# Performance work log

Hardware: AMD Instinct MI355X
Metric: run time of the kernel (lower is better)

The kernel has to match this reference:

```python
import jax, jax.numpy as jnp
import numpy as np

B, I, DI, O, DO = 256, 1152, 8, 10, 16
ROUTING_ITERS = 3


def squash(s):
    # squash along last dim (out_capsule_dim); keepdims version of the
    # module's intended math: v = s * |s|^2 / (1+|s|^2) / |s|
    sq = jnp.sum(s * s, axis=-1, keepdims=True)
    return s * sq / (1.0 + sq) / jnp.sqrt(sq)


def setup_inputs() -> dict:
    key = jax.random.key(0)
    k1, k2 = jax.random.split(key)
    x = jax.random.normal(k1, (B, I, DI), dtype=jnp.float32)
    stdv = 1.0 / np.sqrt(I)
    W = jax.random.uniform(k2, (I, O, DO, DI), dtype=jnp.float32,
                           minval=-stdv, maxval=stdv)
    return {"x": x, "W": W}


def reference(x, W):
    # u_hat[b,i,o,d] = W[i,o,d,k] @ x[b,i,k]
    u_hat = jnp.einsum('iodk,bik->biod', W, x)  # [B, I, O, DO]
    u_det = jax.lax.stop_gradient(u_hat)
    b_ij = jnp.zeros((B, I, O), dtype=u_hat.dtype)
    v = None
    for it in range(ROUTING_ITERS):
        c = jax.nn.softmax(b_ij, axis=2)              # softmax over out caps
        uh = u_hat if it == ROUTING_ITERS - 1 else u_det
        s = jnp.einsum('bio,biod->bod', c, uh)        # [B, O, DO]
        v = squash(s)
        if it < ROUTING_ITERS - 1:
            b_ij = b_ij + jnp.einsum('biod,bod->bio', u_det, v)
    return v  # [B, O, DO]
```

## Files before the change

### kernel.cpp

```cpp
#include <hip/hip_runtime.h>
#include <hip/hip_fp16.h>
#include <math.h>


constexpr int Bc  = 256;
constexpr int Ic  = 1152;
constexpr int Oc  = 10;
constexpr int DOc = 16;
constexpr int ODc = 160;
constexpr int ITILES = 72;

__device__ __forceinline__ float dpp16_sum(float v) {
    int s;
    s = __builtin_amdgcn_update_dpp(0, __float_as_int(v), 0xB1, 0xF, 0xF, true);
    v += __int_as_float(s);
    s = __builtin_amdgcn_update_dpp(0, __float_as_int(v), 0x4E, 0xF, 0xF, true);
    v += __int_as_float(s);
    s = __builtin_amdgcn_update_dpp(0, __float_as_int(v), 0x124, 0xF, 0xF, true);
    v += __int_as_float(s);
    s = __builtin_amdgcn_update_dpp(0, __float_as_int(v), 0x128, 0xF, 0xF, true);
    v += __int_as_float(s);
    return v;
}

__global__ __launch_bounds__(256, 4) void k_uhat(const float* __restrict__ x,
                                                 const float* __restrict__ W,
                                                 __half2* __restrict__ uws,
                                                 float* __restrict__ partial) {
    const int bx    = blockIdx.x;
    const int itile = bx % ITILES;
    const int btile = bx / ITILES;
    const int t     = threadIdx.x;
    const int d     = t & 15;
    const int il    = t >> 4;
    const int w     = t >> 6;
    const int i     = itile * 16 + il;
    const int b0    = btile * 16;

    __shared__ __align__(16) float xs[16 * 128];
    __shared__ __align__(16) float pacc[4 * 16 * ODc];

#pragma unroll
    for (int j = 0; j < 2; ++j) {
        int e  = t + j * 256;
        int bb = e >> 5;
        int r  = e & 31;
        ((float4*)xs)[e] =
            ((const float4*)(x + (size_t)(b0 + bb) * (Ic * 8) + itile * 128))[r];
    }

    float4 wr[20];
    {
        const float4* wp = (const float4*)(W + (((size_t)i * Oc) * DOc + d) * 8);
#pragma unroll
        for (int o = 0; o < Oc; ++o) {
            wr[2 * o]     = wp[o * 32];
            wr[2 * o + 1] = wp[o * 32 + 1];
        }
    }
    __syncthreads();

    const int ch    = i >> 6;
    const int off_t = (i & 63) * 16 + d;

#pragma unroll 1
    for (int bb = 0; bb < 16; ++bb) {
        const int b = b0 + bb;
        const float4 xa = *((const float4*)(xs + bb * 128 + il * 8));
        const float4 xb = *((const float4*)(xs + bb * 128 + il * 8 + 4));
        float u[Oc];
#pragma unroll
        for (int o = 0; o < Oc; ++o) {
            float4 w0 = wr[2 * o], w1 = wr[2 * o + 1];
            u[o] = w0.x * xa.x + w0.y * xa.y + w0.z * xa.z + w0.w * xa.w +
                   w1.x * xb.x + w1.y * xb.y + w1.z * xb.z + w1.w * xb.w;
        }
        __half2* ub = uws + ((size_t)b * 90 + ch * 5) * 1024 + off_t;
#pragma unroll
        for (int op = 0; op < 5; ++op)
            ub[op * 1024] = __floats2half2_rn(u[2 * op], u[2 * op + 1]);
#pragma unroll
        for (int o = 0; o < Oc; ++o) {
            float a = u[o];
            a += __shfl_xor(a, 16);
            a += __shfl_xor(a, 32);
            if ((t & 63) < 16) pacc[(w * 16 + bb) * ODc + o * 16 + d] = a;
        }
    }
    __syncthreads();
#pragma unroll
    for (int j = 0; j < 10; ++j) {
        int e = t + j * 256;
        float s = pacc[e] + pacc[2560 + e] + pacc[5120 + e] + pacc[7680 + e];
        partial[(size_t)itile * (Bc * ODc) + b0 * ODc + e] = s;
    }
}

template <int PASS>
__global__ __launch_bounds__(1024, 8) void k_route(const __half2* __restrict__ uws,
                                                   const float* __restrict__ partial,
                                                   const float* __restrict__ sprev,
                                                   float* __restrict__ vsumg,
                                                   float* __restrict__ spart) {
    const int bx  = blockIdx.x;
    const int b   = bx >> 1;
    const int h   = bx & 1;
    const int t   = threadIdx.x;
    const int d   = t & 15;
    const int wid = t >> 6;

    __shared__ float vs_s[ODc];
    __shared__ float red4[4 * ODc];
    __shared__ float red[16 * ODc];

    if (PASS == 1) {
        const int team = t >> 8;
        const int tt   = t & 255;
        if (tt < ODc) {
            float s = 0.f;
            const float* pb = partial + (size_t)team * 18 * (Bc * ODc) + b * ODc + tt;
#pragma unroll 6
            for (int p = 0; p < 18; ++p) s += pb[(size_t)p * (Bc * ODc)];
            red4[team * ODc + tt] = s;
        }
        __syncthreads();
        if (t < ODc) {
            float s = (red4[t] + red4[ODc + t] + red4[2 * ODc + t] +
                       red4[3 * ODc + t]) * 0.1f;
            float sq = dpp16_sum(s * s);
            float v = s * (sq / ((1.f + sq) * sqrtf(sq)));
            vs_s[t] = v;
            vsumg[b * ODc + t] = v;
        }
    } else {
        if (t < ODc) {
            float s = sprev[b * ODc + t] + sprev[(size_t)(Bc * ODc) + b * ODc + t];
            float sq = dpp16_sum(s * s);
            float v = s * (sq / ((1.f + sq) * sqrtf(sq)));
            vs_s[t] = vsumg[b * ODc + t] + v;
        }
    }
    __syncthreads();

    float vsr[Oc];
#pragma unroll
    for (int o = 0; o < Oc; ++o) vsr[o] = vs_s[o * 16 + d];
    float acc[Oc];
#pragma unroll
    for (int o = 0; o < Oc; ++o) acc[o] = 0.f;

    const __half2* wsb = uws + ((size_t)b * 90 + h * 45) * 1024 + t;
#pragma unroll 1
    for (int ch = 0; ch < 9; ++ch) {
        float uo[Oc];
#pragma unroll
        for (int op = 0; op < 5; ++op) {
            float2 f = __half22float2(wsb[(ch * 5 + op) * 1024]);
            uo[2 * op]     = f.x;
            uo[2 * op + 1] = f.y;
        }
        float c[Oc];
#pragma unroll
        for (int o = 0; o < Oc; ++o) c[o] = dpp16_sum(uo[o] * vsr[o]);
        float m = c[0];
#pragma unroll
        for (int o = 1; o < Oc; ++o) m = fmaxf(m, c[o]);
        float se = 0.f;
#pragma unroll
        for (int o = 0; o < Oc; ++o) {
            c[o] = __expf(c[o] - m);
            se += c[o];
        }
        const float inv = 1.f / se;
#pragma unroll
        for (int o = 0; o < Oc; ++o) acc[o] += (c[o] * inv) * uo[o];
    }
#pragma unroll
    for (int o = 0; o < Oc; ++o) {
        float a = acc[o];
        a += __shfl_xor(a, 16);
        a += __shfl_xor(a, 32);
        if ((t & 63) < 16) red[wid * ODc + o * 16 + d] = a;
    }
    __syncthreads();
    if (t < ODc) {
        float s = 0.f;
#pragma unroll
        for (int w = 0; w < 16; ++w) s += red[w * ODc + t];
        spart[(size_t)h * (Bc * ODc) + b * ODc + t] = s;
    }
}

__global__ __launch_bounds__(192) void k_final(const float* __restrict__ spart,
                                               float* __restrict__ out) {
    const int b = blockIdx.x;
    const int t = threadIdx.x;
    if (t >= ODc) return;
    float s = spart[b * ODc + t] + spart[(size_t)(Bc * ODc) + b * ODc + t];
    float sq = dpp16_sum(s * s);
    float v = s * (sq / ((1.f + sq) * sqrtf(sq)));
    out[(size_t)b * ODc + t] = v;
}

__global__ void __launch_bounds__(1024, 4)
digitcaps_fallback(const float* __restrict__ x, const float* __restrict__ W,
                   float* __restrict__ out) {
    const int b = blockIdx.x, t = threadIdx.x;
    const int lane = t & 63, wid = t >> 6, d = t & 15, iblk = t >> 4;
    __shared__ __align__(16) float xs[Ic * 8];
    __shared__ __align__(16) float red[16 * ODc];
    __shared__ __align__(16) float svec[ODc], vcur[ODc], vsum[ODc];
    {
        const float4* xg = (const float4*)(x + (size_t)b * (Ic * 8));
        float4* xl = (float4*)xs;
        for (int j = t; j < Ic * 2; j += 1024) xl[j] = xg[j];
    }
    if (t < ODc) vsum[t] = 0.f;
    __syncthreads();
    float acc[Oc], vsr[Oc];
    for (int it = 0; it < 3; ++it) {
#pragma unroll
        for (int o = 0; o < Oc; ++o) { acc[o] = 0.f; vsr[o] = vsum[o * 16 + d]; }
#pragma unroll 1
        for (int chk = 0; chk < 18; ++chk) {
            const int i = chk * 64 + iblk;
            const float4 xa = ((const float4*)(xs + i * 8))[0];
            const float4 xb = ((const float4*)(xs + i * 8))[1];
            const float* wb = W + (((size_t)i * Oc) * DOc + d) * 8;
            float uo[Oc];
#pragma unroll
            for (int o = 0; o < Oc; ++o) {
                const float4* wp = (const float4*)(wb + o * 128);
                float4 w0 = wp[0], w1 = wp[1];
                uo[o] = w0.x * xa.x + w0.y * xa.y + w0.z * xa.z + w0.w * xa.w +
                        w1.x * xb.x + w1.y * xb.y + w1.z * xb.z + w1.w * xb.w;
            }
            float cc[Oc];
            if (it > 0) {
#pragma unroll
                for (int o = 0; o < Oc; ++o) cc[o] = dpp16_sum(uo[o] * vsr[o]);
                float m = cc[0];
#pragma unroll
                for (int o = 1; o < Oc; ++o) m = fmaxf(m, cc[o]);
                float se = 0.f;
#pragma unroll
                for (int o = 0; o < Oc; ++o) { cc[o] = __expf(cc[o] - m); se += cc[o]; }
                float inv = 1.f / se;
#pragma unroll
                for (int o = 0; o < Oc; ++o) acc[o] += cc[o] * inv * uo[o];
            } else {
#pragma unroll
                for (int o = 0; o < Oc; ++o) acc[o] += 0.1f * uo[o];
            }
        }
#pragma unroll
        for (int o = 0; o < Oc; ++o) {
            float a = acc[o];
            a += __shfl_xor(a, 16);
            a += __shfl_xor(a, 32);
            if (lane < 16) red[wid * ODc + o * 16 + lane] = a;
        }
        __syncthreads();
        if (t < ODc) {
            float s = 0.f;
#pragma unroll
            for (int w = 0; w < 16; ++w) s += red[w * ODc + t];
            svec[t] = s;
        }
        __syncthreads();
        if (t < Oc) {
            float sq = 0.f;
#pragma unroll
            for (int dd = 0; dd < DOc; ++dd) sq += svec[t * 16 + dd] * svec[t * 16 + dd];
            float sc = sq / ((1.f + sq) * sqrtf(sq));
#pragma unroll
            for (int dd = 0; dd < DOc; ++dd) {
                float v = svec[t * 16 + dd] * sc;
                vcur[t * 16 + dd] = v;
                vsum[t * 16 + dd] += v;
            }
        }
        __syncthreads();
    }
    if (t < ODc) out[(size_t)b * ODc + t] = vcur[t];
}

extern "C" void kernel_launch(void* const* d_in, const int* in_sizes, int n_in,
                              void* d_out, int out_size, void* d_ws, size_t ws_size,
                              hipStream_t stream) {
    (void)in_sizes; (void)n_in; (void)out_size;
    const float* x = (const float*)d_in[0];
    const float* W = (const float*)d_in[1];
    float* out     = (float*)d_out;

    const size_t UWS_B   = (size_t)Bc * 90 * 1024 * sizeof(__half2);
    const size_t PART_B  = (size_t)ITILES * Bc * ODc * sizeof(float);
    const size_t SP1_B   = (size_t)2 * Bc * ODc * sizeof(float);
    const size_t SP2_B   = (size_t)2 * Bc * ODc * sizeof(float);
    const size_t VSUM_B  = (size_t)Bc * ODc * sizeof(float);

    __half2* uws   = (__half2*)d_ws;
    float* partial = (float*)((char*)d_ws + UWS_B);
    float* spart1  = (float*)((char*)d_ws + UWS_B + PART_B);
    float* spart2  = (float*)((char*)d_ws + UWS_B + PART_B + SP1_B);
    float* vsumg   = (float*)((char*)d_ws + UWS_B + PART_B + SP1_B + SP2_B);

    if (ws_size >= UWS_B + PART_B + SP1_B + SP2_B + VSUM_B) {
        hipLaunchKernelGGL(k_uhat, dim3(ITILES * 16), dim3(256), 0, stream,
                           x, W, uws, partial);
        hipLaunchKernelGGL((k_route<1>), dim3(512), dim3(1024), 0, stream,
                           uws, partial, nullptr, vsumg, spart1);
        hipLaunchKernelGGL((k_route<2>), dim3(512), dim3(1024), 0, stream,
                           uws, nullptr, spart1, vsumg, spart2);
        hipLaunchKernelGGL(k_final, dim3(Bc), dim3(192), 0, stream,
                           spart2, out);
    } else {
        hipLaunchKernelGGL(digitcaps_fallback, dim3(Bc), dim3(1024), 0, stream,
                           x, W, out);
    }
}
```

Measured before the change: 150.4 us.

## Recompute u_hat per routing pass instead of storing fp16 workspace

Removes the materialised fp16 u_hat workspace. Each routing iteration now recomputes u_hat from x and W in registers, builds the softmax-weighted partial sums per i-tile, and a reduce kernel turns them into v and the accumulated v sum. This avoids writing and reading back about 94 MB of u_hat per pass and computes the routing weights from full fp32 values. In exchange it adds recomputation, more kernel launches, and 72-way partial reductions per pass.

Measured after the change: 261.8 us. 74.1% more time.

```diff
diff --git a/kernel.cpp b/kernel.cpp
--- a/kernel.cpp
+++ b/kernel.cpp
@@ -1,5 +1,4 @@
 #include <hip/hip_runtime.h>
-#include <hip/hip_fp16.h>
 #include <math.h>
 
 
@@ -23,10 +22,9 @@
     return v;
 }
 
-__global__ __launch_bounds__(256, 4) void k_uhat(const float* __restrict__ x,
-                                                 const float* __restrict__ W,
-                                                 __half2* __restrict__ uws,
-                                                 float* __restrict__ partial) {
+__global__ __launch_bounds__(256, 4) void k_uhat_p0(const float* __restrict__ x,
+                                                    const float* __restrict__ W,
+                                                    float* __restrict__ partial) {
     const int bx    = blockIdx.x;
     const int itile = bx % ITILES;
     const int btile = bx / ITILES;
@@ -60,12 +58,8 @@
     }
     __syncthreads();
 
-    const int ch    = i >> 6;
-    const int off_t = (i & 63) * 16 + d;
-
 #pragma unroll 1
     for (int bb = 0; bb < 16; ++bb) {
-        const int b = b0 + bb;
         const float4 xa = *((const float4*)(xs + bb * 128 + il * 8));
         const float4 xb = *((const float4*)(xs + bb * 128 + il * 8 + 4));
         float u[Oc];
@@ -75,10 +69,6 @@
             u[o] = w0.x * xa.x + w0.y * xa.y + w0.z * xa.z + w0.w * xa.w +
                    w1.x * xb.x + w1.y * xb.y + w1.z * xb.z + w1.w * xb.w;
         }
-        __half2* ub = uws + ((size_t)b * 90 + ch * 5) * 1024 + off_t;
-#pragma unroll
-        for (int op = 0; op < 5; ++op)
-            ub[op * 1024] = __floats2half2_rn(u[2 * op], u[2 * op + 1]);
 #pragma unroll
         for (int o = 0; o < Oc; ++o) {
             float a = u[o];
@@ -96,72 +86,63 @@
     }
 }
 
-template <int PASS>
-__global__ __launch_bounds__(1024, 8) void k_route(const __half2* __restrict__ uws,
-                                                   const float* __restrict__ partial,
-                                                   const float* __restrict__ sprev,
-                                                   float* __restrict__ vsumg,
-                                                   float* __restrict__ spart) {
-    const int bx  = blockIdx.x;
-    const int b   = bx >> 1;
-    const int h   = bx & 1;
-    const int t   = threadIdx.x;
-    const int d   = t & 15;
-    const int wid = t >> 6;
-
-    __shared__ float vs_s[ODc];
-    __shared__ float red4[4 * ODc];
-    __shared__ float red[16 * ODc];
-
-    if (PASS == 1) {
-        const int team = t >> 8;
-        const int tt   = t & 255;
-        if (tt < ODc) {
-            float s = 0.f;
-            const float* pb = partial + (size_t)team * 18 * (Bc * ODc) + b * ODc + tt;
-#pragma unroll 6
-            for (int p = 0; p < 18; ++p) s += pb[(size_t)p * (Bc * ODc)];
-            red4[team * ODc + tt] = s;
-        }
-        __syncthreads();
-        if (t < ODc) {
-            float s = (red4[t] + red4[ODc + t] + red4[2 * ODc + t] +
-                       red4[3 * ODc + t]) * 0.1f;
-            float sq = dpp16_sum(s * s);
-            float v = s * (sq / ((1.f + sq) * sqrtf(sq)));
-            vs_s[t] = v;
-            vsumg[b * ODc + t] = v;
-        }
-    } else {
-        if (t < ODc) {
-            float s = sprev[b * ODc + t] + sprev[(size_t)(Bc * ODc) + b * ODc + t];
-            float sq = dpp16_sum(s * s);
-            float v = s * (sq / ((1.f + sq) * sqrtf(sq)));
-            vs_s[t] = vsumg[b * ODc + t] + v;
-        }
-    }
-    __syncthreads();
-
-    float vsr[Oc];
-#pragma unroll
-    for (int o = 0; o < Oc; ++o) vsr[o] = vs_s[o * 16 + d];
-    float acc[Oc];
-#pragma unroll
-    for (int o = 0; o < Oc; ++o) acc[o] = 0.f;
-
-    const __half2* wsb = uws + ((size_t)b * 90 + h * 45) * 1024 + t;
+__global__ __launch_bounds__(256, 3) void k_iter(const float* __restrict__ x,
+                                                 const float* __restrict__ W,
+                                                 const float* __restrict__ vsum,
+                                                 float* __restrict__ spart) {
+    const int bx    = blockIdx.x;
+    const int itile = bx % ITILES;
+    const int btile = bx / ITILES;
+    const int t     = threadIdx.x;
+    const int d     = t & 15;
+    const int il    = t >> 4;
+    const int w     = t >> 6;
+    const int i     = itile * 16 + il;
+    const int b0    = btile * 16;
+
+    __shared__ __align__(16) float xs[16 * 128];
+    __shared__ __align__(16) float pacc[4 * 16 * ODc];
+
+#pragma unroll
+    for (int j = 0; j < 2; ++j) {
+        int e  = t + j * 256;
+        int bb = e >> 5;
+        int r  = e & 31;
+        ((float4*)xs)[e] =
+            ((const float4*)(x + (size_t)(b0 + bb) * (Ic * 8) + itile * 128))[r];
+    }
+
+    float4 wr[20];
+    {
+        const float4* wp = (const float4*)(W + (((size_t)i * Oc) * DOc + d) * 8);
+#pragma unroll
+        for (int o = 0; o < Oc; ++o) {
+            wr[2 * o]     = wp[o * 32];
+            wr[2 * o + 1] = wp[o * 32 + 1];
+        }
+    }
+    __syncthreads();
+
 #pragma unroll 1
-    for (int ch = 0; ch < 9; ++ch) {
-        float uo[Oc];
-#pragma unroll
-        for (int op = 0; op < 5; ++op) {
-            float2 f = __half22float2(wsb[(ch * 5 + op) * 1024]);
-            uo[2 * op]     = f.x;
-            uo[2 * op + 1] = f.y;
+    for (int bb = 0; bb < 16; ++bb) {
+        const float* vb = vsum + (size_t)(b0 + bb) * 256 + d * 16;
+        const float4 va = *((const float4*)vb);
+        const float4 vc = *((const float4*)(vb + 4));
+        const float2 ve = *((const float2*)(vb + 8));
+        float vr[Oc] = {va.x, va.y, va.z, va.w, vc.x, vc.y, vc.z, vc.w, ve.x, ve.y};
+
+        const float4 xa = *((const float4*)(xs + bb * 128 + il * 8));
+        const float4 xb = *((const float4*)(xs + bb * 128 + il * 8 + 4));
+        float u[Oc];
+#pragma unroll
+        for (int o = 0; o < Oc; ++o) {
+            float4 w0 = wr[2 * o], w1 = wr[2 * o + 1];
+            u[o] = w0.x * xa.x + w0.y * xa.y + w0.z * xa.z + w0.w * xa.w +
+                   w1.x * xb.x + w1.y * xb.y + w1.z * xb.z + w1.w * xb.w;
         }
         float c[Oc];
 #pragma unroll
-        for (int o = 0; o < Oc; ++o) c[o] = dpp16_sum(uo[o] * vsr[o]);
+        for (int o = 0; o < Oc; ++o) c[o] = dpp16_sum(u[o] * vr[o]);
         float m = c[0];
 #pragma unroll
         for (int o = 1; o < Oc; ++o) m = fmaxf(m, c[o]);
@@ -173,33 +154,44 @@
         }
         const float inv = 1.f / se;
 #pragma unroll
-        for (int o = 0; o < Oc; ++o) acc[o] += (c[o] * inv) * uo[o];
-    }
-#pragma unroll
-    for (int o = 0; o < Oc; ++o) {
-        float a = acc[o];
-        a += __shfl_xor(a, 16);
-        a += __shfl_xor(a, 32);
-        if ((t & 63) < 16) red[wid * ODc + o * 16 + d] = a;
-    }
-    __syncthreads();
-    if (t < ODc) {
-        float s = 0.f;
-#pragma unroll
-        for (int w = 0; w < 16; ++w) s += red[w * ODc + t];
-        spart[(size_t)h * (Bc * ODc) + b * ODc + t] = s;
-    }
-}
-
-__global__ __launch_bounds__(192) void k_final(const float* __restrict__ spart,
-                                               float* __restrict__ out) {
+        for (int o = 0; o < Oc; ++o) {
+            float a = (c[o] * inv) * u[o];
+            a += __shfl_xor(a, 16);
+            a += __shfl_xor(a, 32);
+            if ((t & 63) < 16) pacc[(w * 16 + bb) * ODc + o * 16 + d] = a;
+        }
+    }
+    __syncthreads();
+#pragma unroll
+    for (int j = 0; j < 10; ++j) {
+        int e = t + j * 256;
+        float s = pacc[e] + pacc[2560 + e] + pacc[5120 + e] + pacc[7680 + e];
+        spart[(size_t)itile * (Bc * ODc) + b0 * ODc + e] = s;
+    }
+}
+
+template <int P>
+__global__ __launch_bounds__(192) void k_reduce(const float* __restrict__ part,
+                                                float* __restrict__ vsumg,
+                                                float* __restrict__ out) {
     const int b = blockIdx.x;
     const int t = threadIdx.x;
     if (t >= ODc) return;
-    float s = spart[b * ODc + t] + spart[(size_t)(Bc * ODc) + b * ODc + t];
+    float s = 0.f;
+    const float* pb = part + (size_t)b * ODc + t;
+#pragma unroll
+    for (int p = 0; p < ITILES; ++p) s += pb[(size_t)p * (Bc * ODc)];
+    if (P == 0) s *= 0.1f;
     float sq = dpp16_sum(s * s);
     float v = s * (sq / ((1.f + sq) * sqrtf(sq)));
-    out[(size_t)b * ODc + t] = v;
+    if constexpr (P == 2) {
+        out[(size_t)b * ODc + t] = v;
+    } else {
+        const int o = t >> 4, dd = t & 15;
+        float* vp = vsumg + (size_t)b * 256 + dd * 16 + o;
+        if constexpr (P == 0) *vp = v;
+        else                  *vp += v;
+    }
 }
 
 __global__ void __launch_bounds__(1024, 4)
@@ -293,27 +285,25 @@
     const float* W = (const float*)d_in[1];
     float* out     = (float*)d_out;
 
-    const size_t UWS_B   = (size_t)Bc * 90 * 1024 * sizeof(__half2);
-    const size_t PART_B  = (size_t)ITILES * Bc * ODc * sizeof(float);
-    const size_t SP1_B   = (size_t)2 * Bc * ODc * sizeof(float);
-    const size_t SP2_B   = (size_t)2 * Bc * ODc * sizeof(float);
-    const size_t VSUM_B  = (size_t)Bc * ODc * sizeof(float);
-
-    __half2* uws   = (__half2*)d_ws;
-    float* partial = (float*)((char*)d_ws + UWS_B);
-    float* spart1  = (float*)((char*)d_ws + UWS_B + PART_B);
-    float* spart2  = (float*)((char*)d_ws + UWS_B + PART_B + SP1_B);
-    float* vsumg   = (float*)((char*)d_ws + UWS_B + PART_B + SP1_B + SP2_B);
-
-    if (ws_size >= UWS_B + PART_B + SP1_B + SP2_B + VSUM_B) {
-        hipLaunchKernelGGL(k_uhat, dim3(ITILES * 16), dim3(256), 0, stream,
-                           x, W, uws, partial);
-        hipLaunchKernelGGL((k_route<1>), dim3(512), dim3(1024), 0, stream,
-                           uws, partial, nullptr, vsumg, spart1);
-        hipLaunchKernelGGL((k_route<2>), dim3(512), dim3(1024), 0, stream,
-                           uws, nullptr, spart1, vsumg, spart2);
-        hipLaunchKernelGGL(k_final, dim3(Bc), dim3(192), 0, stream,
-                           spart2, out);
+    const size_t PART_B = (size_t)ITILES * Bc * ODc * sizeof(float);
+    const size_t VS_B   = (size_t)Bc * 256 * sizeof(float);
+
+    float* partial = (float*)d_ws;
+    float* vsumg   = (float*)((char*)d_ws + PART_B);
+
+    if (ws_size >= PART_B + VS_B) {
+        hipLaunchKernelGGL(k_uhat_p0, dim3(ITILES * 16), dim3(256), 0, stream,
+                           x, W, partial);
+        hipLaunchKernelGGL((k_reduce<0>), dim3(Bc), dim3(192), 0, stream,
+                           partial, vsumg, nullptr);
+        hipLaunchKernelGGL(k_iter, dim3(ITILES * 16), dim3(256), 0, stream,
+                           x, W, vsumg, partial);
+        hipLaunchKernelGGL((k_reduce<1>), dim3(Bc), dim3(192), 0, stream,
+                           partial, vsumg, nullptr);
+        hipLaunchKernelGGL(k_iter, dim3(ITILES * 16), dim3(256), 0, stream,
+                           x, W, vsumg, partial);
+        hipLaunchKernelGGL((k_reduce<2>), dim3(Bc), dim3(192), 0, stream,
+                           partial, nullptr, out);
     } else {
         hipLaunchKernelGGL(digitcaps_fallback, dim3(Bc), dim3(1024), 0, stream,
                            x, W, out);
```
